# Kernel tuning notes

Hardware: AMD Instinct MI355X
Metric: run time of the kernel (lower is better)

## Reference

```python
import jax, jax.numpy as jnp
import numpy as np

N_ATOMS = 100_000
N_PAIRS = 6_400_000
BOX_L = 50.0


def setup_inputs() -> dict:
    key = jax.random.key(0)
    k1, k2, k3, k4 = jax.random.split(key, 4)
    # coords uniformly inside the box [0, BOX_L)^3
    coords = jax.random.uniform(k1, (N_ATOMS, 3), dtype=jnp.float32) * BOX_L
    # pairs: i random, j = i + random offset in [1, N-1] mod N  (guarantees i != j)
    i = jax.random.randint(k2, (N_PAIRS,), 0, N_ATOMS)
    off = jax.random.randint(k3, (N_PAIRS,), 1, N_ATOMS)
    j = (i + off) % N_ATOMS
    pairs = jnp.stack([i, j], axis=1).astype(jnp.int64)
    # cubic periodic box (invertible 3x3)
    box = (jnp.eye(3, dtype=jnp.float32) * BOX_L)
    charges = jax.random.normal(k4, (N_ATOMS,), dtype=jnp.float32)
    prefac = jnp.float32(138.935)   # Coulomb constant (kJ/mol nm e^-2 style)
    cutoff = jnp.float32(10.0)
    return {"coords": coords, "pairs": pairs, "box": box, "charges": charges,
            "prefac": prefac, "cutoff": cutoff, "do_shift": 1}


def reference(coords, pairs, box, charges, prefac, cutoff, do_shift):
    idx_i = pairs[:, 0]
    idx_j = pairs[:, 1]
    drVecs = coords[idx_i] - coords[idx_j]          # [P, 3] gather + subtract
    boxInv = jnp.linalg.inv(box)                    # [3, 3]
    dsVecs = drVecs @ boxInv                        # fractional coords [P, 3]
    dsVecsPBC = dsVecs - jnp.floor(dsVecs + 0.5)    # minimum-image wrap
    drVecsPBC = dsVecsPBC @ box                     # back to cartesian [P, 3]
    dr = jnp.linalg.norm(drVecsPBC, axis=1)         # [P]
    mask = dr <= cutoff
    rinv = 1.0 / dr
    if do_shift:
        rinv = rinv - 1.0 / cutoff
    ene = charges[idx_i] * charges[idx_j] * rinv    # [P]
    return jnp.sum(ene * mask) * prefac
```

## Files before the change

kernel.cpp:

```cpp
#include <hip/hip_runtime.h>
#include <hip/hip_fp16.h>


constexpr int TPB = 256;

constexpr int CHUNK_SHIFT = 13;
constexpr int CHUNK       = 1 << CHUNK_SHIFT;
constexpr int NCHUNK_MAX  = 15;
constexpr int NB_MAX      = 256;

constexpr int S_TPB = 512;
constexpr int S_PPT = 16;
constexpr int S_PPB = S_TPB * S_PPT;
constexpr int S_I4  = S_PPB / 2;
constexpr int S_UI  = S_I4 / S_TPB;

constexpr int C_TPB   = 1024;
constexpr int C_SPLIT = 4;
constexpr int C_NW    = C_TPB / 64;

constexpr size_t WS_ACC   = 0;
constexpr size_t WS_PAR   = 16;
constexpr size_t WS_PARTS = 4096;
constexpr size_t WS_TABLE = 36864;

__device__ __forceinline__ void compute_par(const float* __restrict__ box,
                                            const float* __restrict__ cutoff_p,
                                            const int* __restrict__ do_shift_p,
                                            float* par) {
    float b00 = box[0], b01 = box[1], b02 = box[2];
    float b10 = box[3], b11 = box[4], b12 = box[5];
    float b20 = box[6], b21 = box[7], b22 = box[8];
    float det = b00*(b11*b22 - b12*b21)
              - b01*(b10*b22 - b12*b20)
              + b02*(b10*b21 - b11*b20);
    float id = 1.0f / det;
    par[0] =  (b11*b22 - b12*b21) * id;
    par[1] = -(b01*b22 - b02*b21) * id;
    par[2] =  (b01*b12 - b02*b11) * id;
    par[3] = -(b10*b22 - b12*b20) * id;
    par[4] =  (b00*b22 - b02*b20) * id;
    par[5] = -(b00*b12 - b02*b10) * id;
    par[6] =  (b10*b21 - b11*b20) * id;
    par[7] = -(b00*b21 - b01*b20) * id;
    par[8] =  (b00*b11 - b01*b10) * id;
    float cut = *cutoff_p;
    par[9]  = cut * cut;
    par[10] = (*do_shift_p) ? (1.0f / cut) : 0.0f;
    constexpr float S = 1.0f / 65536.0f;
    par[11] = b00*S; par[12] = b01*S; par[13] = b02*S;
    par[14] = b10*S; par[15] = b11*S; par[16] = b12*S;
    par[17] = b20*S; par[18] = b21*S; par[19] = b22*S;
    float offd = fabsf(b01) + fabsf(b02) + fabsf(b10)
               + fabsf(b12) + fabsf(b20) + fabsf(b21);
    par[20] = (offd == 0.0f) ? 1.0f : 0.0f;
}


__global__ __launch_bounds__(S_TPB)
void scatter_kernel(const int4* __restrict__ pairs4, int npair2, int nchunk,
                    int nbucket, int nsb,
                    const float* __restrict__ coords,
                    const float* __restrict__ charges,
                    const float* __restrict__ box,
                    const float* __restrict__ cutoff_p,
                    const int* __restrict__ do_shift_p,
                    uint2* __restrict__ qatoms, int natoms,
                    unsigned* __restrict__ tableT,
                    unsigned* __restrict__ bdata) {
    __shared__ __align__(16) unsigned ordered[S_PPB];
    __shared__ unsigned hist[NB_MAX];
    __shared__ unsigned sA[NB_MAX], sB[NB_MAX];

    int tid = threadIdx.x;
    int blk = blockIdx.x;

    {
        float par[21];
        compute_par(box, cutoff_p, do_shift_p, par);
        int per = (natoms + nsb - 1) / nsb;
        int a0 = blk * per;
        int a1 = min(natoms, a0 + per);
        for (int i = a0 + tid; i < a1; i += S_TPB) {
            float x = coords[3*i], y = coords[3*i+1], z = coords[3*i+2];
            float sx = x*par[0] + y*par[3] + z*par[6];
            float sy = x*par[1] + y*par[4] + z*par[7];
            float sz = x*par[2] + y*par[5] + z*par[8];
            unsigned qx = (unsigned)__float2int_rn(sx * 65536.0f) & 0xFFFFu;
            unsigned qy = (unsigned)__float2int_rn(sy * 65536.0f) & 0xFFFFu;
            unsigned qz = (unsigned)__float2int_rn(sz * 65536.0f) & 0xFFFFu;
            unsigned qc = (unsigned)__half_as_ushort(__float2half(charges[i]));
            qatoms[i] = make_uint2(qx | (qy << 16), qz | (qc << 16));
        }
    }

    for (int t = tid; t < NB_MAX; t += S_TPB) hist[t] = 0u;
    __syncthreads();

    int base4 = blk * S_I4;
    unsigned k[S_PPT];
    unsigned bs[S_PPT];
#pragma unroll
    for (int u = 0; u < S_UI; ++u) {
        int i4 = base4 + u * S_TPB + tid;
        bool v = (i4 < npair2);
        int4 pp = v ? pairs4[i4] : make_int4(0, 0, 0, 0);
        int u2 = 2 * u;
        if (v) {
            int b0 = (pp.x >> CHUNK_SHIFT) * nchunk + (pp.y >> CHUNK_SHIFT);
            int b1 = (pp.z >> CHUNK_SHIFT) * nchunk + (pp.w >> CHUNK_SHIFT);
            k[u2]     = ((unsigned)(pp.x & (CHUNK-1)) << 16) | (unsigned)(pp.y & (CHUNK-1));
            k[u2 + 1] = ((unsigned)(pp.z & (CHUNK-1)) << 16) | (unsigned)(pp.w & (CHUNK-1));
            unsigned s0 = atomicAdd(&hist[b0], 1u);
            bs[u2] = (unsigned)b0 | (s0 << 8);
            unsigned s1 = atomicAdd(&hist[b1], 1u);
            bs[u2 + 1] = (unsigned)b1 | (s1 << 8);
        } else {
            bs[u2] = 0xFFFFFFFFu; bs[u2 + 1] = 0xFFFFFFFFu;
        }
    }
    __syncthreads();

    unsigned *pa = sA, *pb = sB;
    if (tid < NB_MAX) pa[tid] = hist[tid];
    __syncthreads();
    for (int d = 1; d < NB_MAX; d <<= 1) {
        if (tid < NB_MAX) {
            unsigned v = pa[tid];
            if (tid >= d) v += pa[tid - d];
            pb[tid] = v;
        }
        __syncthreads();
        unsigned* t = pa; pa = pb; pb = t;
    }
    if (tid <= nbucket) {
        unsigned excl = (tid == 0) ? 0u : pa[tid - 1];
        tableT[(size_t)tid * nsb + blk] = excl;
        if (tid < nbucket) hist[tid] = excl;
    }
    __syncthreads();

#pragma unroll
    for (int u = 0; u < S_PPT; ++u) {
        if (bs[u] != 0xFFFFFFFFu) {
            unsigned b = bs[u] & 0xFFu;
            unsigned slot = hist[b] + (bs[u] >> 8);
            ordered[slot] = k[u];
        }
    }
    __syncthreads();

    unsigned total = pa[nbucket - 1];
    unsigned* dst = bdata + (size_t)blk * S_PPB;
    unsigned n4 = total >> 2;
    const uint4* o4 = (const uint4*)ordered;
    for (unsigned i = tid; i < n4; i += S_TPB)
        ((uint4*)dst)[i] = o4[i];
    for (unsigned i = (n4 << 2) + tid; i < total; i += S_TPB)
        dst[i] = ordered[i];
}


template<bool DIAG>
__device__ __forceinline__ float pair_ener(const uint2* tA, const uint2* tB,
                                           unsigned key, const float* P,
                                           bool valid) {
    uint2 ri = tA[key >> 16];
    uint2 rj = tB[key & 0xFFFFu];
    float dx = (float)(short)(ri.x - rj.x);
    float dy = (float)(short)((ri.x >> 16) - (rj.x >> 16));
    float dz = (float)(short)(ri.y - rj.y);
    float px, py, pz;
    if (DIAG) {
        px = dx * P[11]; py = dy * P[15]; pz = dz * P[19];
    } else {
        px = dx*P[11] + dy*P[14] + dz*P[17];
        py = dx*P[12] + dy*P[15] + dz*P[18];
        pz = dx*P[13] + dy*P[16] + dz*P[19];
    }
    float r2 = px*px + py*py + pz*pz;
    float rinv = rsqrtf(r2);
    float qi = __half2float(__ushort_as_half((unsigned short)(ri.y >> 16)));
    float qj = __half2float(__ushort_as_half((unsigned short)(rj.y >> 16)));
    float e = qi * qj * (rinv - P[10]);
    return (valid && r2 <= P[9]) ? e : 0.0f;
}

template<bool DIAG>
__device__ double walk(const unsigned* __restrict__ bdata,
                       const unsigned* __restrict__ rowB,
                       const unsigned* __restrict__ rowB1,
                       int sA0, int cnt, int lane,
                       const uint2* tA, const uint2* tB, const float* P) {
    double lsum0 = 0.0, lsum1 = 0.0;
    for (int batch = 0; batch < cnt; batch += 64) {
        int bc = min(64, cnt - batch);
        unsigned o0v = 0u, lnv = 0u;
        if (lane < bc) {
            int s = sA0 + batch + lane;
            unsigned a0 = rowB[s];
            unsigned a1 = rowB1[s];
            o0v = a0;
            lnv = a1 - a0;
        }
        for (int kk = 0; kk < bc; kk += 4) {
            unsigned off0 = (unsigned)__shfl((int)o0v, kk);
            unsigned len0 = (kk     < bc) ? (unsigned)__shfl((int)lnv, kk)     : 0u;
            unsigned off1 = (unsigned)__shfl((int)o0v, kk + 1);
            unsigned len1 = (kk + 1 < bc) ? (unsigned)__shfl((int)lnv, kk + 1) : 0u;
            unsigned off2 = (unsigned)__shfl((int)o0v, kk + 2);
            unsigned len2 = (kk + 2 < bc) ? (unsigned)__shfl((int)lnv, kk + 2) : 0u;
            unsigned off3 = (unsigned)__shfl((int)o0v, kk + 3);
            unsigned len3 = (kk + 3 < bc) ? (unsigned)__shfl((int)lnv, kk + 3) : 0u;
            size_t base0 = (size_t)(sA0 + batch + kk    ) * S_PPB + off0;
            size_t base1 = (size_t)(sA0 + batch + kk + 1) * S_PPB + off1;
            size_t base2 = (size_t)(sA0 + batch + kk + 2) * S_PPB + off2;
            size_t base3 = (size_t)(sA0 + batch + kk + 3) * S_PPB + off3;
            unsigned k0 = (lane < (int)len0) ? bdata[base0 + lane] : 0u;
            unsigned k1 = (lane < (int)len1) ? bdata[base1 + lane] : 0u;
            unsigned k2 = (lane < (int)len2) ? bdata[base2 + lane] : 0u;
            unsigned k3 = (lane < (int)len3) ? bdata[base3 + lane] : 0u;
            lsum0 += (double)pair_ener<DIAG>(tA, tB, k0, P, lane < (int)len0);
            lsum1 += (double)pair_ener<DIAG>(tA, tB, k1, P, lane < (int)len1);
            lsum0 += (double)pair_ener<DIAG>(tA, tB, k2, P, lane < (int)len2);
            lsum1 += (double)pair_ener<DIAG>(tA, tB, k3, P, lane < (int)len3);
            if (len0 > 64u) for (unsigned e = 64u + lane; e < len0; e += 64u)
                lsum0 += (double)pair_ener<DIAG>(tA, tB, bdata[base0 + e], P, true);
            if (len1 > 64u) for (unsigned e = 64u + lane; e < len1; e += 64u)
                lsum1 += (double)pair_ener<DIAG>(tA, tB, bdata[base1 + e], P, true);
            if (len2 > 64u) for (unsigned e = 64u + lane; e < len2; e += 64u)
                lsum0 += (double)pair_ener<DIAG>(tA, tB, bdata[base2 + e], P, true);
            if (len3 > 64u) for (unsigned e = 64u + lane; e < len3; e += 64u)
                lsum1 += (double)pair_ener<DIAG>(tA, tB, bdata[base3 + e], P, true);
        }
    }
    return lsum0 + lsum1;
}

__global__ __launch_bounds__(C_TPB)
void bucket_compute(const unsigned* __restrict__ bdata,
                    const unsigned* __restrict__ tableT, int nsb,
                    const uint2* __restrict__ qatoms, int natoms, int nchunk,
                    const float* __restrict__ box,
                    const float* __restrict__ cutoff_p,
                    const int* __restrict__ do_shift_p,
                    double* __restrict__ parts) {
    __shared__ uint2 tA[CHUNK];
    __shared__ uint2 tB[CHUNK];
    __shared__ double wsum[C_NW];
    __shared__ float sP[21];

    if (threadIdx.x == 0) compute_par(box, cutoff_p, do_shift_p, sP);

    int b    = blockIdx.x / C_SPLIT;
    int part = blockIdx.x - b * C_SPLIT;
    int bx = b / nchunk, by = b - bx * nchunk;
    int gx = bx << CHUNK_SHIFT, gy = by << CHUNK_SHIFT;

    for (int t = threadIdx.x; t < CHUNK; t += C_TPB) {
        int ga = gx + t;
        tA[t] = (ga < natoms) ? qatoms[ga] : make_uint2(0u, 0u);
        int gb = gy + t;
        tB[t] = (gb < natoms) ? qatoms[gb] : make_uint2(0u, 0u);
    }
    __syncthreads();

    float P[21];
#pragma unroll
    for (int k = 0; k < 21; ++k) P[k] = sP[k];

    int s0 = (int)(((long long)part * nsb) / C_SPLIT);
    int s1 = (int)(((long long)(part + 1) * nsb) / C_SPLIT);
    int lane = threadIdx.x & 63;
    int wid  = threadIdx.x >> 6;

    int nseg = s1 - s0;
    int spw  = (nseg + C_NW - 1) / C_NW;
    int sA0  = s0 + wid * spw;
    int cnt  = min(spw, s1 - sA0);
    if (cnt < 0) cnt = 0;

    const unsigned* rowB  = tableT + (size_t)b * nsb;
    const unsigned* rowB1 = tableT + (size_t)(b + 1) * nsb;

    double lsum = (P[20] != 0.0f)
        ? walk<true >(bdata, rowB, rowB1, sA0, cnt, lane, tA, tB, P)
        : walk<false>(bdata, rowB, rowB1, sA0, cnt, lane, tA, tB, P);

#pragma unroll
    for (int off = 32; off > 0; off >>= 1)
        lsum += __shfl_down(lsum, off);

    if (lane == 0) wsum[wid] = lsum;
    __syncthreads();
    if (threadIdx.x == 0) {
        double s = 0.0;
#pragma unroll
        for (int w = 0; w < C_NW; ++w) s += wsum[w];
        parts[blockIdx.x] = s;
    }
}

__global__ void finalize_bucket(const double* __restrict__ parts, int n,
                                const float* __restrict__ prefac_p,
                                const float* __restrict__ box,
                                const float* __restrict__ cutoff_p,
                                const int* __restrict__ do_shift_p,
                                const float* __restrict__ coords,
                                const float* __restrict__ charges,
                                const int* __restrict__ pairs, int npairs,
                                float* __restrict__ out) {
    __shared__ double sh[4];
    double s = 0.0;
    for (int i = threadIdx.x; i < n; i += 256) s += parts[i];
#pragma unroll
    for (int off = 32; off > 0; off >>= 1) s += __shfl_down(s, off);
    int lane = threadIdx.x & 63, wid = threadIdx.x >> 6;
    if (lane == 0) sh[wid] = s;
    __syncthreads();
    if (threadIdx.x == 0) {
        double tot = sh[0] + sh[1] + sh[2] + sh[3];
        if (npairs & 1) {
            float par[21];
            compute_par(box, cutoff_p, do_shift_p, par);
            int ii = pairs[2*(npairs-1)], jj = pairs[2*(npairs-1)+1];
            float dx = coords[3*ii]-coords[3*jj];
            float dy = coords[3*ii+1]-coords[3*jj+1];
            float dz = coords[3*ii+2]-coords[3*jj+2];
            float sx = dx*par[0]+dy*par[3]+dz*par[6];
            float sy = dx*par[1]+dy*par[4]+dz*par[7];
            float sz = dx*par[2]+dy*par[5]+dz*par[8];
            sx -= floorf(sx+0.5f); sy -= floorf(sy+0.5f); sz -= floorf(sz+0.5f);
            float px = (sx*par[11]+sy*par[14]+sz*par[17])*65536.0f;
            float py = (sx*par[12]+sy*par[15]+sz*par[18])*65536.0f;
            float pz = (sx*par[13]+sy*par[16]+sz*par[19])*65536.0f;
            float r2 = px*px+py*py+pz*pz;
            float e = charges[ii]*charges[jj]*(rsqrtf(r2)-par[10]);
            if (r2 <= par[9]) tot += (double)e;
        }
        out[0] = (float)(tot * (double)(*prefac_p));
    }
}


__global__ void setup_kernel(const float* __restrict__ box,
                             const float* __restrict__ cutoff_p,
                             const int* __restrict__ do_shift_p,
                             double* __restrict__ acc,
                             float* __restrict__ par) {
    if (threadIdx.x == 0 && blockIdx.x == 0) {
        *acc = 0.0;
        compute_par(box, cutoff_p, do_shift_p, par);
    }
}

__device__ __forceinline__ float pair_e_f(float4 ai, float4 aj, const float* P) {
    float dx = ai.x - aj.x, dy = ai.y - aj.y, dz = ai.z - aj.z;
    float sx = dx*P[0] + dy*P[3] + dz*P[6];
    float sy = dx*P[1] + dy*P[4] + dz*P[7];
    float sz = dx*P[2] + dy*P[5] + dz*P[8];
    sx -= floorf(sx + 0.5f);
    sy -= floorf(sy + 0.5f);
    sz -= floorf(sz + 0.5f);
    float px = (sx*P[11] + sy*P[14] + sz*P[17]) * 65536.0f;
    float py = (sx*P[12] + sy*P[15] + sz*P[18]) * 65536.0f;
    float pz = (sx*P[13] + sy*P[16] + sz*P[19]) * 65536.0f;
    float r2 = px*px + py*py + pz*pz;
    float rinv = rsqrtf(r2);
    float e = ai.w * aj.w * (rinv - P[10]);
    return (r2 <= P[9]) ? e : 0.0f;
}

__global__ __launch_bounds__(TPB)
void coulomb_direct(const int2* __restrict__ pairs, int npairs,
                    const float* __restrict__ coords,
                    const float* __restrict__ charges,
                    const float* __restrict__ par,
                    double* __restrict__ acc) {
    float P[21];
#pragma unroll
    for (int k = 0; k < 21; ++k) P[k] = par[k];
    double lsum = 0.0;
    int tid = blockIdx.x * blockDim.x + threadIdx.x;
    int stride = gridDim.x * blockDim.x;
    for (int p = tid; p < npairs; p += stride) {
        int2 pr = pairs[p];
        float4 a = make_float4(coords[3*pr.x], coords[3*pr.x+1], coords[3*pr.x+2], charges[pr.x]);
        float4 c = make_float4(coords[3*pr.y], coords[3*pr.y+1], coords[3*pr.y+2], charges[pr.y]);
        lsum += (double)pair_e_f(a, c, P);
    }
#pragma unroll
    for (int off = 32; off > 0; off >>= 1)
        lsum += __shfl_down(lsum, off);
    __shared__ double wsum[TPB / 64];
    int lane = threadIdx.x & 63;
    int wid  = threadIdx.x >> 6;
    if (lane == 0) wsum[wid] = lsum;
    __syncthreads();
    if (threadIdx.x == 0) {
        double s = 0.0;
#pragma unroll
        for (int w = 0; w < TPB / 64; ++w) s += wsum[w];
        atomicAdd(acc, s);
    }
}

__global__ void finalize_kernel(const double* __restrict__ acc,
                                const float* __restrict__ prefac_p,
                                float* __restrict__ out) {
    if (threadIdx.x == 0 && blockIdx.x == 0)
        out[0] = (float)(*acc * (double)(*prefac_p));
}

extern "C" void kernel_launch(void* const* d_in, const int* in_sizes, int n_in,
                              void* d_out, int out_size, void* d_ws, size_t ws_size,
                              hipStream_t stream) {
    const float* coords   = (const float*)d_in[0];
    const int*   pairs    = (const int*)d_in[1];
    const float* box      = (const float*)d_in[2];
    const float* charges  = (const float*)d_in[3];
    const float* prefac   = (const float*)d_in[4];
    const float* cutoff   = (const float*)d_in[5];
    const int*   do_shift = (const int*)d_in[6];
    float* out = (float*)d_out;

    int natoms = in_sizes[0] / 3;
    int npairs = in_sizes[1] / 2;
    int npair2 = npairs / 2;
    int npairs_even = npair2 * 2;

    int nchunk  = (natoms + CHUNK - 1) >> CHUNK_SHIFT;
    int nbucket = nchunk * nchunk;
    int nsb     = (npairs_even + S_PPB - 1) / S_PPB;

    size_t off_table  = WS_TABLE;
    size_t table_b    = (size_t)(nbucket + 1) * nsb * sizeof(unsigned);
    size_t off_qatoms = (off_table + table_b + 255) & ~(size_t)255;
    size_t off_bdata  = (off_qatoms + (size_t)natoms * sizeof(uint2) + 255) & ~(size_t)255;
    size_t need       = off_bdata + (size_t)nsb * S_PPB * sizeof(unsigned);

    int cblocks = nbucket * C_SPLIT;
    bool use_buckets = (nchunk <= NCHUNK_MAX) && (nbucket <= NB_MAX - 2) &&
                       (nsb >= 1) && (ws_size >= need) && (cblocks <= 4096);

    if (use_buckets) {
        double*   parts  = (double*)((char*)d_ws + WS_PARTS);
        unsigned* tableT = (unsigned*)((char*)d_ws + off_table);
        uint2*    qatoms = (uint2*)((char*)d_ws + off_qatoms);
        unsigned* bdata  = (unsigned*)((char*)d_ws + off_bdata);

        scatter_kernel<<<nsb, S_TPB, 0, stream>>>(
            (const int4*)pairs, npair2, nchunk, nbucket, nsb,
            coords, charges, box, cutoff, do_shift, qatoms, natoms,
            tableT, bdata);

        bucket_compute<<<cblocks, C_TPB, 0, stream>>>(
            bdata, tableT, nsb, qatoms, natoms, nchunk,
            box, cutoff, do_shift, parts);

        finalize_bucket<<<1, 256, 0, stream>>>(
            parts, cblocks, prefac, box, cutoff, do_shift,
            coords, charges, pairs, npairs, out);
    } else {
        double* acc = (double*)((char*)d_ws + WS_ACC);
        float*  par = (float*)((char*)d_ws + WS_PAR);
        setup_kernel<<<1, 64, 0, stream>>>(box, cutoff, do_shift, acc, par);
        int blocks = (npairs + TPB - 1) / TPB;
        if (blocks > 2048) blocks = 2048;
        coulomb_direct<<<blocks, TPB, 0, stream>>>(
            (const int2*)pairs, npairs, coords, charges, par, acc);
        finalize_kernel<<<1, 64, 0, stream>>>(acc, prefac, out);
    }
}
```

Before: 56.98 us.

## Replace prefix-sum bucket scatter with fixed-capacity padded buckets plus overflow list

The scatter kernel now writes pairs into fixed-capacity (64-slot) per-bucket shared-memory slots padded with sentinels, dropping the block-level prefix scan, offset table and variable-length segment walk. The compute kernel reads dense padded bucket arrays with uint4 loads and skips sentinel keys, and bucket overflows go to a global list processed by a separate overflow kernel. This removes the table indirection and the irregular per-segment loops, but adds padding traffic, a memset, an extra kernel launch and sentinel work.

```diff
diff --git a/kernel.cpp b/kernel.cpp
--- a/kernel.cpp
+++ b/kernel.cpp
@@ -6,8 +6,12 @@
 
 constexpr int CHUNK_SHIFT = 13;
 constexpr int CHUNK       = 1 << CHUNK_SHIFT;
-constexpr int NCHUNK_MAX  = 15;
-constexpr int NB_MAX      = 256;
+constexpr int NCHUNK_MAX  = 13;
+constexpr int NB_MAX      = 169;
+constexpr int CAP         = 64;
+constexpr unsigned SENT   = 0xFFFFFFFFu;
+constexpr int OVF_CAP     = 262144;
+constexpr int OV_BLOCKS   = 8;
 
 constexpr int S_TPB = 512;
 constexpr int S_PPT = 16;
@@ -16,13 +20,14 @@
 constexpr int S_UI  = S_I4 / S_TPB;
 
 constexpr int C_TPB   = 1024;
-constexpr int C_SPLIT = 4;
+constexpr int C_SPLIT = 3;
 constexpr int C_NW    = C_TPB / 64;
 
 constexpr size_t WS_ACC   = 0;
 constexpr size_t WS_PAR   = 16;
+constexpr size_t WS_OVCNT = 2048;
 constexpr size_t WS_PARTS = 4096;
-constexpr size_t WS_TABLE = 36864;
+constexpr size_t WS_DYN   = 36864;
 
 __device__ __forceinline__ void compute_par(const float* __restrict__ box,
                                             const float* __restrict__ cutoff_p,
@@ -66,14 +71,17 @@
                     const float* __restrict__ cutoff_p,
                     const int* __restrict__ do_shift_p,
                     uint2* __restrict__ qatoms, int natoms,
-                    unsigned* __restrict__ tableT,
+                    unsigned* __restrict__ ovfcnt, uint2* __restrict__ ovflist,
                     unsigned* __restrict__ bdata) {
-    __shared__ __align__(16) unsigned ordered[S_PPB];
-    __shared__ unsigned hist[NB_MAX];
-    __shared__ unsigned sA[NB_MAX], sB[NB_MAX];
+    __shared__ __align__(16) unsigned ordered[NB_MAX * CAP];
+    __shared__ unsigned hist[NB_MAX + 7];
+    __shared__ uint2 sovf[1024];
+    __shared__ unsigned sovf_cnt, gbase;
 
     int tid = threadIdx.x;
     int blk = blockIdx.x;
+    int lane = tid & 63;
+    int wid  = tid >> 6;
 
     {
         float par[21];
@@ -94,79 +102,64 @@
         }
     }
 
-    for (int t = tid; t < NB_MAX; t += S_TPB) hist[t] = 0u;
+    for (int t = tid; t < NB_MAX * CAP; t += S_TPB) ordered[t] = SENT;
+    for (int t = tid; t < NB_MAX + 7; t += S_TPB) hist[t] = 0u;
+    if (tid == 0) sovf_cnt = 0u;
     __syncthreads();
 
     int base4 = blk * S_I4;
-    unsigned k[S_PPT];
-    unsigned bs[S_PPT];
 #pragma unroll
     for (int u = 0; u < S_UI; ++u) {
         int i4 = base4 + u * S_TPB + tid;
-        bool v = (i4 < npair2);
-        int4 pp = v ? pairs4[i4] : make_int4(0, 0, 0, 0);
-        int u2 = 2 * u;
-        if (v) {
+        if (i4 < npair2) {
+            int4 pp = pairs4[i4];
             int b0 = (pp.x >> CHUNK_SHIFT) * nchunk + (pp.y >> CHUNK_SHIFT);
             int b1 = (pp.z >> CHUNK_SHIFT) * nchunk + (pp.w >> CHUNK_SHIFT);
-            k[u2]     = ((unsigned)(pp.x & (CHUNK-1)) << 16) | (unsigned)(pp.y & (CHUNK-1));
-            k[u2 + 1] = ((unsigned)(pp.z & (CHUNK-1)) << 16) | (unsigned)(pp.w & (CHUNK-1));
+            unsigned k0 = ((unsigned)(pp.x & (CHUNK-1)) << 16) | (unsigned)(pp.y & (CHUNK-1));
+            unsigned k1 = ((unsigned)(pp.z & (CHUNK-1)) << 16) | (unsigned)(pp.w & (CHUNK-1));
             unsigned s0 = atomicAdd(&hist[b0], 1u);
-            bs[u2] = (unsigned)b0 | (s0 << 8);
+            if (s0 < (unsigned)CAP) {
+                ordered[b0 * CAP + s0] = k0;
+            } else {
+                unsigned o = atomicAdd(&sovf_cnt, 1u);
+                if (o < 1024u) sovf[o] = make_uint2((unsigned)b0, k0);
+                else { unsigned g = atomicAdd(ovfcnt, 1u);
+                       if (g < (unsigned)OVF_CAP) ovflist[g] = make_uint2((unsigned)b0, k0); }
+            }
             unsigned s1 = atomicAdd(&hist[b1], 1u);
-            bs[u2 + 1] = (unsigned)b1 | (s1 << 8);
-        } else {
-            bs[u2] = 0xFFFFFFFFu; bs[u2 + 1] = 0xFFFFFFFFu;
+            if (s1 < (unsigned)CAP) {
+                ordered[b1 * CAP + s1] = k1;
+            } else {
+                unsigned o = atomicAdd(&sovf_cnt, 1u);
+                if (o < 1024u) sovf[o] = make_uint2((unsigned)b1, k1);
+                else { unsigned g = atomicAdd(ovfcnt, 1u);
+                       if (g < (unsigned)OVF_CAP) ovflist[g] = make_uint2((unsigned)b1, k1); }
+            }
         }
     }
     __syncthreads();
 
-    unsigned *pa = sA, *pb = sB;
-    if (tid < NB_MAX) pa[tid] = hist[tid];
-    __syncthreads();
-    for (int d = 1; d < NB_MAX; d <<= 1) {
-        if (tid < NB_MAX) {
-            unsigned v = pa[tid];
-            if (tid >= d) v += pa[tid - d];
-            pb[tid] = v;
-        }
-        __syncthreads();
-        unsigned* t = pa; pa = pb; pb = t;
-    }
-    if (tid <= nbucket) {
-        unsigned excl = (tid == 0) ? 0u : pa[tid - 1];
-        tableT[(size_t)tid * nsb + blk] = excl;
-        if (tid < nbucket) hist[tid] = excl;
-    }
-    __syncthreads();
-
-#pragma unroll
-    for (int u = 0; u < S_PPT; ++u) {
-        if (bs[u] != 0xFFFFFFFFu) {
-            unsigned b = bs[u] & 0xFFu;
-            unsigned slot = hist[b] + (bs[u] >> 8);
-            ordered[slot] = k[u];
-        }
-    }
-    __syncthreads();
-
-    unsigned total = pa[nbucket - 1];
-    unsigned* dst = bdata + (size_t)blk * S_PPB;
-    unsigned n4 = total >> 2;
-    const uint4* o4 = (const uint4*)ordered;
-    for (unsigned i = tid; i < n4; i += S_TPB)
-        ((uint4*)dst)[i] = o4[i];
-    for (unsigned i = (n4 << 2) + tid; i < total; i += S_TPB)
-        dst[i] = ordered[i];
+    size_t bstride = (size_t)nsb * CAP;
+    for (int f = wid; f < nbucket; f += S_TPB / 64) {
+        unsigned v = ordered[f * CAP + lane];
+        bdata[(size_t)f * bstride + (size_t)blk * CAP + lane] = v;
+    }
+
+    unsigned c = min(sovf_cnt, 1024u);
+    if (tid == 0 && c) gbase = atomicAdd(ovfcnt, c);
+    __syncthreads();
+    for (unsigned t = tid; t < c; t += S_TPB) {
+        unsigned g = gbase + t;
+        if (g < (unsigned)OVF_CAP) ovflist[g] = sovf[t];
+    }
 }
 
 
 template<bool DIAG>
 __device__ __forceinline__ float pair_ener(const uint2* tA, const uint2* tB,
-                                           unsigned key, const float* P,
-                                           bool valid) {
-    uint2 ri = tA[key >> 16];
-    uint2 rj = tB[key & 0xFFFFu];
+                                           unsigned key, const float* P) {
+    uint2 ri = tA[(key >> 16) & (CHUNK - 1)];
+    uint2 rj = tB[key & (CHUNK - 1)];
     float dx = (float)(short)(ri.x - rj.x);
     float dy = (float)(short)((ri.x >> 16) - (rj.x >> 16));
     float dz = (float)(short)(ri.y - rj.y);
@@ -183,63 +176,26 @@
     float qi = __half2float(__ushort_as_half((unsigned short)(ri.y >> 16)));
     float qj = __half2float(__ushort_as_half((unsigned short)(rj.y >> 16)));
     float e = qi * qj * (rinv - P[10]);
-    return (valid && r2 <= P[9]) ? e : 0.0f;
+    return (key != SENT && r2 <= P[9]) ? e : 0.0f;
 }
 
 template<bool DIAG>
-__device__ double walk(const unsigned* __restrict__ bdata,
-                       const unsigned* __restrict__ rowB,
-                       const unsigned* __restrict__ rowB1,
-                       int sA0, int cnt, int lane,
-                       const uint2* tA, const uint2* tB, const float* P) {
-    double lsum0 = 0.0, lsum1 = 0.0;
-    for (int batch = 0; batch < cnt; batch += 64) {
-        int bc = min(64, cnt - batch);
-        unsigned o0v = 0u, lnv = 0u;
-        if (lane < bc) {
-            int s = sA0 + batch + lane;
-            unsigned a0 = rowB[s];
-            unsigned a1 = rowB1[s];
-            o0v = a0;
-            lnv = a1 - a0;
-        }
-        for (int kk = 0; kk < bc; kk += 4) {
-            unsigned off0 = (unsigned)__shfl((int)o0v, kk);
-            unsigned len0 = (kk     < bc) ? (unsigned)__shfl((int)lnv, kk)     : 0u;
-            unsigned off1 = (unsigned)__shfl((int)o0v, kk + 1);
-            unsigned len1 = (kk + 1 < bc) ? (unsigned)__shfl((int)lnv, kk + 1) : 0u;
-            unsigned off2 = (unsigned)__shfl((int)o0v, kk + 2);
-            unsigned len2 = (kk + 2 < bc) ? (unsigned)__shfl((int)lnv, kk + 2) : 0u;
-            unsigned off3 = (unsigned)__shfl((int)o0v, kk + 3);
-            unsigned len3 = (kk + 3 < bc) ? (unsigned)__shfl((int)lnv, kk + 3) : 0u;
-            size_t base0 = (size_t)(sA0 + batch + kk    ) * S_PPB + off0;
-            size_t base1 = (size_t)(sA0 + batch + kk + 1) * S_PPB + off1;
-            size_t base2 = (size_t)(sA0 + batch + kk + 2) * S_PPB + off2;
-            size_t base3 = (size_t)(sA0 + batch + kk + 3) * S_PPB + off3;
-            unsigned k0 = (lane < (int)len0) ? bdata[base0 + lane] : 0u;
-            unsigned k1 = (lane < (int)len1) ? bdata[base1 + lane] : 0u;
-            unsigned k2 = (lane < (int)len2) ? bdata[base2 + lane] : 0u;
-            unsigned k3 = (lane < (int)len3) ? bdata[base3 + lane] : 0u;
-            lsum0 += (double)pair_ener<DIAG>(tA, tB, k0, P, lane < (int)len0);
-            lsum1 += (double)pair_ener<DIAG>(tA, tB, k1, P, lane < (int)len1);
-            lsum0 += (double)pair_ener<DIAG>(tA, tB, k2, P, lane < (int)len2);
-            lsum1 += (double)pair_ener<DIAG>(tA, tB, k3, P, lane < (int)len3);
-            if (len0 > 64u) for (unsigned e = 64u + lane; e < len0; e += 64u)
-                lsum0 += (double)pair_ener<DIAG>(tA, tB, bdata[base0 + e], P, true);
-            if (len1 > 64u) for (unsigned e = 64u + lane; e < len1; e += 64u)
-                lsum1 += (double)pair_ener<DIAG>(tA, tB, bdata[base1 + e], P, true);
-            if (len2 > 64u) for (unsigned e = 64u + lane; e < len2; e += 64u)
-                lsum0 += (double)pair_ener<DIAG>(tA, tB, bdata[base2 + e], P, true);
-            if (len3 > 64u) for (unsigned e = 64u + lane; e < len3; e += 64u)
-                lsum1 += (double)pair_ener<DIAG>(tA, tB, bdata[base3 + e], P, true);
-        }
-    }
-    return lsum0 + lsum1;
+__device__ double dense_walk(const unsigned* __restrict__ src,
+                             int w0, int w1, int tid,
+                             const uint2* tA, const uint2* tB, const float* P) {
+    double l0 = 0.0, l1 = 0.0;
+    for (int w = w0 + tid * 4; w < w1; w += C_TPB * 4) {
+        uint4 kv = *reinterpret_cast<const uint4*>(src + w);
+        l0 += (double)pair_ener<DIAG>(tA, tB, kv.x, P);
+        l1 += (double)pair_ener<DIAG>(tA, tB, kv.y, P);
+        l0 += (double)pair_ener<DIAG>(tA, tB, kv.z, P);
+        l1 += (double)pair_ener<DIAG>(tA, tB, kv.w, P);
+    }
+    return l0 + l1;
 }
 
 __global__ __launch_bounds__(C_TPB)
-void bucket_compute(const unsigned* __restrict__ bdata,
-                    const unsigned* __restrict__ tableT, int nsb,
+void bucket_compute(const unsigned* __restrict__ bdata, int nsb,
                     const uint2* __restrict__ qatoms, int natoms, int nchunk,
                     const float* __restrict__ box,
                     const float* __restrict__ cutoff_p,
@@ -269,35 +225,77 @@
 #pragma unroll
     for (int k = 0; k < 21; ++k) P[k] = sP[k];
 
-    int s0 = (int)(((long long)part * nsb) / C_SPLIT);
-    int s1 = (int)(((long long)(part + 1) * nsb) / C_SPLIT);
+    int span = nsb * CAP;
+    const unsigned* src = bdata + (size_t)b * span;
+    int w0 = (int)(((long long)span * part) / C_SPLIT) & ~3;
+    int w1 = (part == C_SPLIT - 1) ? span
+             : (int)(((long long)span * (part + 1)) / C_SPLIT) & ~3;
+
+    double lsum = (P[20] != 0.0f)
+        ? dense_walk<true >(src, w0, w1, threadIdx.x, tA, tB, P)
+        : dense_walk<false>(src, w0, w1, threadIdx.x, tA, tB, P);
+
+#pragma unroll
+    for (int off = 32; off > 0; off >>= 1)
+        lsum += __shfl_down(lsum, off);
+
     int lane = threadIdx.x & 63;
     int wid  = threadIdx.x >> 6;
-
-    int nseg = s1 - s0;
-    int spw  = (nseg + C_NW - 1) / C_NW;
-    int sA0  = s0 + wid * spw;
-    int cnt  = min(spw, s1 - sA0);
-    if (cnt < 0) cnt = 0;
-
-    const unsigned* rowB  = tableT + (size_t)b * nsb;
-    const unsigned* rowB1 = tableT + (size_t)(b + 1) * nsb;
-
-    double lsum = (P[20] != 0.0f)
-        ? walk<true >(bdata, rowB, rowB1, sA0, cnt, lane, tA, tB, P)
-        : walk<false>(bdata, rowB, rowB1, sA0, cnt, lane, tA, tB, P);
-
+    if (lane == 0) wsum[wid] = lsum;
+    __syncthreads();
+    if (threadIdx.x == 0) {
+        double s = 0.0;
+#pragma unroll
+        for (int w = 0; w < C_NW; ++w) s += wsum[w];
+        parts[blockIdx.x] = s;
+    }
+}
+
+__global__ void overflow_kernel(const uint2* __restrict__ ovflist,
+                                const unsigned* __restrict__ ovfcnt,
+                                const uint2* __restrict__ qatoms, int nchunk,
+                                const float* __restrict__ box,
+                                const float* __restrict__ cutoff_p,
+                                const int* __restrict__ do_shift_p,
+                                double* __restrict__ parts, int cblocks) {
+    float P[21];
+    compute_par(box, cutoff_p, do_shift_p, P);
+    int n = (int)min(*ovfcnt, (unsigned)OVF_CAP);
+    double lsum = 0.0;
+    for (int t = blockIdx.x * blockDim.x + threadIdx.x; t < n;
+         t += gridDim.x * blockDim.x) {
+        uint2 ov = ovflist[t];
+        int b = (int)ov.x;
+        unsigned key = ov.y;
+        int ig = ((b / nchunk) << CHUNK_SHIFT) | (int)((key >> 16) & (CHUNK - 1));
+        int jg = ((b % nchunk) << CHUNK_SHIFT) | (int)(key & (CHUNK - 1));
+        uint2 ri = qatoms[ig];
+        uint2 rj = qatoms[jg];
+        float dx = (float)(short)(ri.x - rj.x);
+        float dy = (float)(short)((ri.x >> 16) - (rj.x >> 16));
+        float dz = (float)(short)(ri.y - rj.y);
+        float px = dx*P[11] + dy*P[14] + dz*P[17];
+        float py = dx*P[12] + dy*P[15] + dz*P[18];
+        float pz = dx*P[13] + dy*P[16] + dz*P[19];
+        float r2 = px*px + py*py + pz*pz;
+        float qi = __half2float(__ushort_as_half((unsigned short)(ri.y >> 16)));
+        float qj = __half2float(__ushort_as_half((unsigned short)(rj.y >> 16)));
+        float e = qi * qj * (rsqrtf(r2) - P[10]);
+        lsum += (double)((r2 <= P[9]) ? e : 0.0f);
+    }
 #pragma unroll
     for (int off = 32; off > 0; off >>= 1)
         lsum += __shfl_down(lsum, off);
-
+    __shared__ double wsum[TPB / 64];
+    int lane = threadIdx.x & 63;
+    int wid  = threadIdx.x >> 6;
     if (lane == 0) wsum[wid] = lsum;
     __syncthreads();
     if (threadIdx.x == 0) {
         double s = 0.0;
 #pragma unroll
-        for (int w = 0; w < C_NW; ++w) s += wsum[w];
-        parts[blockIdx.x] = s;
+        for (int w = 0; w < TPB / 64; ++w) s += wsum[w];
+        parts[cblocks + blockIdx.x] = s;
     }
 }
 
@@ -433,33 +431,41 @@
     int nbucket = nchunk * nchunk;
     int nsb     = (npairs_even + S_PPB - 1) / S_PPB;
 
-    size_t off_table  = WS_TABLE;
-    size_t table_b    = (size_t)(nbucket + 1) * nsb * sizeof(unsigned);
-    size_t off_qatoms = (off_table + table_b + 255) & ~(size_t)255;
+    size_t off_qatoms = WS_DYN;
     size_t off_bdata  = (off_qatoms + (size_t)natoms * sizeof(uint2) + 255) & ~(size_t)255;
-    size_t need       = off_bdata + (size_t)nsb * S_PPB * sizeof(unsigned);
+    size_t bdata_b    = (size_t)nbucket * nsb * CAP * sizeof(unsigned);
+    size_t off_ovf    = (off_bdata + bdata_b + 255) & ~(size_t)255;
+    size_t need       = off_ovf + (size_t)OVF_CAP * sizeof(uint2);
 
     int cblocks = nbucket * C_SPLIT;
-    bool use_buckets = (nchunk <= NCHUNK_MAX) && (nbucket <= NB_MAX - 2) &&
-                       (nsb >= 1) && (ws_size >= need) && (cblocks <= 4096);
+    bool use_buckets = (nchunk <= NCHUNK_MAX) && (nsb >= 1) &&
+                       (ws_size >= need) &&
+                       (cblocks + OV_BLOCKS <= 4000);
 
     if (use_buckets) {
+        unsigned* ovfcnt = (unsigned*)((char*)d_ws + WS_OVCNT);
         double*   parts  = (double*)((char*)d_ws + WS_PARTS);
-        unsigned* tableT = (unsigned*)((char*)d_ws + off_table);
         uint2*    qatoms = (uint2*)((char*)d_ws + off_qatoms);
         unsigned* bdata  = (unsigned*)((char*)d_ws + off_bdata);
+        uint2*    ovflist= (uint2*)((char*)d_ws + off_ovf);
+
+        hipMemsetAsync(ovfcnt, 0, sizeof(unsigned), stream);
 
         scatter_kernel<<<nsb, S_TPB, 0, stream>>>(
             (const int4*)pairs, npair2, nchunk, nbucket, nsb,
             coords, charges, box, cutoff, do_shift, qatoms, natoms,
-            tableT, bdata);
+            ovfcnt, ovflist, bdata);
 
         bucket_compute<<<cblocks, C_TPB, 0, stream>>>(
-            bdata, tableT, nsb, qatoms, natoms, nchunk,
+            bdata, nsb, qatoms, natoms, nchunk,
             box, cutoff, do_shift, parts);
 
+        overflow_kernel<<<OV_BLOCKS, TPB, 0, stream>>>(
+            ovflist, ovfcnt, qatoms, nchunk, box, cutoff, do_shift,
+            parts, cblocks);
+
         finalize_bucket<<<1, 256, 0, stream>>>(
-            parts, cblocks, prefac, box, cutoff, do_shift,
+            parts, cblocks + OV_BLOCKS, prefac, box, cutoff, do_shift,
             coords, charges, pairs, npairs, out);
     } else {
         double* acc = (double*)((char*)d_ws + WS_ACC);
```

New measurement: 81.24 us. 42.6% more time.
